# Kernel optimization log

Measured on AMD Instinct MI355X. Metric: run time of the kernel, lower is better.

The kernel has to match this reference:

```python
import jax, jax.numpy as jnp
import numpy as np

B, S, D = 4, 2048, 1024

def setup_inputs() -> dict:
    key = jax.random.key(0)
    ks = jax.random.split(key, 9)
    q = jax.random.normal(ks[0], (B, S, D), dtype=jnp.float32)
    k = jax.random.normal(ks[1], (B, S, D), dtype=jnp.float32)
    v = jax.random.normal(ks[2], (B, S, D), dtype=jnp.float32)
    # Dense layer params (Glorot-ish scale), bias included like keras Dense
    sc = 1.0 / np.sqrt(D)
    Wq = jax.random.normal(ks[3], (D, D), dtype=jnp.float32) * sc
    Wk = jax.random.normal(ks[4], (D, D), dtype=jnp.float32) * sc
    Wv = jax.random.normal(ks[5], (D, D), dtype=jnp.float32) * sc
    bq = jnp.zeros((D,), dtype=jnp.float32)
    bk = jnp.zeros((D,), dtype=jnp.float32)
    bv = jnp.zeros((D,), dtype=jnp.float32)
    # causal mask: 1 where attention is forbidden (future positions)
    mask = jnp.triu(jnp.ones((S, S), dtype=jnp.float32), k=1)
    return {"q": q, "k": k, "v": v, "mask": mask,
            "Wq": Wq, "bq": bq, "Wk": Wk, "bk": bk, "Wv": Wv, "bv": bv}

def reference(q, k, v, mask, Wq, bq, Wk, bk, Wv, bv):
    WQ = q @ Wq + bq                      # [B,S,D]
    WK = k @ Wk + bk
    WV = v @ Wv + bv
    d_k = jnp.asarray(WK.shape[-1], dtype=jnp.float32)
    scores = jnp.einsum('bqd,bkd->bqk', WQ, WK) / jnp.sqrt(d_k)  # [B,S,S]
    scores = scores + mask * (-1e9)
    attn = jax.nn.softmax(scores, axis=-1)
    return jnp.einsum('bqk,bkd->bqd', attn, WV)
```

## Files before the change

kernel.cpp:

```cpp
#include <hip/hip_runtime.h>
#include <math.h>

#define S_LEN 2048
#define D_DIM 1024
#define NB    4

typedef __bf16 bf16_t;
typedef __bf16 bf16x8 __attribute__((ext_vector_type(8)));
typedef float  f32x4  __attribute__((ext_vector_type(4)));
typedef unsigned int   u32;
typedef unsigned short u16;
typedef unsigned int   u32x4 __attribute__((ext_vector_type(4)));

#define BM 128
#define BN 128
#define BK 64

__device__ __forceinline__ u16 f2b_bits(float x) {
    bf16_t h = (bf16_t)x;
    return *(u16*)&h;
}

__device__ __forceinline__ void async16(const void* g, void* l) {
    __builtin_amdgcn_global_load_lds(
        (__attribute__((address_space(1))) const void*)g,
        (__attribute__((address_space(3))) void*)l, 16, 0, 0);
}

#define BAR_RAW() asm volatile("s_barrier" ::: "memory")

__device__ __forceinline__ void gemm_bt_core(
    const bf16_t* __restrict__ A, const bf16_t* __restrict__ Bt,
    int lda, int ldb, int m0, int n0, int kTiles, f32x4 (&acc)[4][4])
{
    __shared__ __attribute__((aligned(16))) bf16_t lA[BM * BK];
    __shared__ __attribute__((aligned(16))) bf16_t lB[BN * BK];
    const int t    = threadIdx.x;
    const int w    = t >> 6;
    const int lane = t & 63;
    const int wr   = w >> 1, wc = w & 1;
    const int srow   = lane >> 3;
    const int kb_src = ((lane & 7) ^ (lane >> 3)) * 8;
    const int fr = lane & 15, fq = lane >> 4;
    const int fof0 = (((0 * 4 + fq) ^ (fr & 7)) * 8);
    const int fof1 = (((1 * 4 + fq) ^ (fr & 7)) * 8);
    const bf16_t* paB0 = lA + (wr * 64 + fr) * BK + fof0;
    const bf16_t* paB1 = lA + (wr * 64 + fr) * BK + fof1;
    const bf16_t* pbB0 = lB + (wc * 64 + fr) * BK + fof0;
    const bf16_t* pbB1 = lB + (wc * 64 + fr) * BK + fof1;
    bf16_t* ldsA = lA + (w * 32) * BK;
    bf16_t* ldsB = lB + (w * 32) * BK;
    const bf16_t* gA = A  + (long)(m0 + w * 32 + srow) * lda + kb_src;
    const bf16_t* gB = Bt + (long)(n0 + w * 32 + srow) * ldb + kb_src;

#pragma unroll
    for (int mt = 0; mt < 4; ++mt)
#pragma unroll
        for (int nt = 0; nt < 4; ++nt)
            acc[mt][nt] = f32x4{0.f, 0.f, 0.f, 0.f};

    for (int kt = 0; kt < kTiles; ++kt) {
        const long k0 = (long)kt * BK;
#pragma unroll
        for (int i = 0; i < 4; ++i) {
            async16(gA + k0 + (long)(i * 8) * lda, ldsA + i * 8 * BK);
            async16(gB + k0 + (long)(i * 8) * ldb, ldsB + i * 8 * BK);
        }
        asm volatile("s_waitcnt vmcnt(0)" ::: "memory");
        __syncthreads();
#pragma unroll
        for (int h = 0; h < 2; ++h) {
            const bf16_t* pa = h ? paB1 : paB0;
            const bf16_t* pb = h ? pbB1 : pbB0;
            bf16x8 af[4], bfv[4];
#pragma unroll
            for (int mt = 0; mt < 4; ++mt)
                af[mt] = *(const bf16x8*)(pa + mt * 16 * BK);
#pragma unroll
            for (int nt = 0; nt < 4; ++nt)
                bfv[nt] = *(const bf16x8*)(pb + nt * 16 * BK);
#pragma unroll
            for (int mt = 0; mt < 4; ++mt)
#pragma unroll
                for (int nt = 0; nt < 4; ++nt)
                    acc[mt][nt] = __builtin_amdgcn_mfma_f32_16x16x32_bf16(
                        af[mt], bfv[nt], acc[mt][nt], 0, 0, 0);
        }
        __syncthreads();
    }
}

__device__ __forceinline__ void gemm_bt_dbuf8(
    const bf16_t* __restrict__ A, const bf16_t* __restrict__ Bt,
    int lda, int ldb, int m0, int n0, int kTiles, f32x4 (&acc)[4][2])
{
    __shared__ __attribute__((aligned(16))) bf16_t lA[2][BM * BK];
    __shared__ __attribute__((aligned(16))) bf16_t lB[2][BN * BK];
    const int t    = threadIdx.x;
    const int w    = t >> 6;
    const int lane = t & 63;
    const int wr   = w >> 2, wc = w & 3;
    const int srow   = lane >> 3;
    const int kb_src = ((lane & 7) ^ srow) * 8;
    const int fr = lane & 15, fq = lane >> 4;
    const int fof0 = (((0 * 4 + fq) ^ (fr & 7)) * 8);
    const int fof1 = (((1 * 4 + fq) ^ (fr & 7)) * 8);
    const int aO0 = (wr * 64 + fr) * BK + fof0;
    const int aO1 = (wr * 64 + fr) * BK + fof1;
    const int bO0 = (wc * 32 + fr) * BK + fof0;
    const int bO1 = (wc * 32 + fr) * BK + fof1;
    const int sOf = (w * 8) * BK;
    const bf16_t* gA = A  + (long)(m0 + w * 8 + srow) * lda + kb_src;
    const bf16_t* gB = Bt + (long)(n0 + w * 8 + srow) * ldb + kb_src;

#pragma unroll
    for (int mt = 0; mt < 4; ++mt)
#pragma unroll
        for (int nt = 0; nt < 2; ++nt)
            acc[mt][nt] = f32x4{0.f, 0.f, 0.f, 0.f};

#pragma unroll
    for (int i = 0; i < 2; ++i) {
        async16(gA + (long)(i * 64) * lda, &lA[0][sOf + i * 64 * BK]);
        async16(gB + (long)(i * 64) * ldb, &lB[0][sOf + i * 64 * BK]);
    }

    for (int kt = 0; kt < kTiles; ++kt) {
        const int cur = kt & 1, nxt = cur ^ 1;
        if (kt + 1 < kTiles) {
            const long k1 = (long)(kt + 1) * BK;
#pragma unroll
            for (int i = 0; i < 2; ++i) {
                async16(gA + k1 + (long)(i * 64) * lda, &lA[nxt][sOf + i * 64 * BK]);
                async16(gB + k1 + (long)(i * 64) * ldb, &lB[nxt][sOf + i * 64 * BK]);
            }
            asm volatile("s_waitcnt vmcnt(4)" ::: "memory");
        } else {
            asm volatile("s_waitcnt vmcnt(0)" ::: "memory");
        }
        BAR_RAW();
        const bf16_t* lac = lA[cur];
        const bf16_t* lbc = lB[cur];
#pragma unroll
        for (int h = 0; h < 2; ++h) {
            const bf16_t* pa = lac + (h ? aO1 : aO0);
            const bf16_t* pb = lbc + (h ? bO1 : bO0);
            bf16x8 af[4], bfv[2];
#pragma unroll
            for (int mt = 0; mt < 4; ++mt)
                af[mt] = *(const bf16x8*)(pa + mt * 16 * BK);
#pragma unroll
            for (int nt = 0; nt < 2; ++nt)
                bfv[nt] = *(const bf16x8*)(pb + nt * 16 * BK);
#pragma unroll
            for (int mt = 0; mt < 4; ++mt)
#pragma unroll
                for (int nt = 0; nt < 2; ++nt)
                    acc[mt][nt] = __builtin_amdgcn_mfma_f32_16x16x32_bf16(
                        af[mt], bfv[nt], acc[mt][nt], 0, 0, 0);
        }
        BAR_RAW();
    }
}

__global__ __launch_bounds__(256) void k_f2b(
    const float* __restrict__ q, const float* __restrict__ k,
    const float* __restrict__ v, bf16_t* __restrict__ Xb)
{
    const int z = blockIdx.z;
    const float* src = (z == 0) ? q : ((z == 1) ? k : v);
    bf16_t* dst = Xb + (long)z * ((long)NB * S_LEN * D_DIM);
    const long i = (long)blockIdx.x * blockDim.x + threadIdx.x;
    float4 a = ((const float4*)src)[i];
    u32 lo = (u32)f2b_bits(a.x) | ((u32)f2b_bits(a.y) << 16);
    u32 hi = (u32)f2b_bits(a.z) | ((u32)f2b_bits(a.w) << 16);
    ((uint2*)(dst))[i] = make_uint2(lo, hi);
}

__global__ __launch_bounds__(256) void k_tw(
    const float* __restrict__ Wq, const float* __restrict__ Wk,
    const float* __restrict__ Wv, bf16_t* __restrict__ Wt)
{
    __shared__ u32 tile[64][33];
    const int z = blockIdx.z;
    const float* W = (z == 0) ? Wq : ((z == 1) ? Wk : Wv);
    bf16_t* T = Wt + (long)z * D_DIM * D_DIM;
    const int t = threadIdx.x;
    const int k0 = blockIdx.x * 64, n0 = blockIdx.y * 64;
#pragma unroll
    for (int rr = 0; rr < 4; ++rr) {
        const int kr = (t >> 4) + rr * 16;
        const int nq = (t & 15) * 4;
        float4 f = *(const float4*)(W + (long)(k0 + kr) * D_DIM + n0 + nq);
        tile[kr][(nq >> 1)]     = (u32)f2b_bits(f.x) | ((u32)f2b_bits(f.y) << 16);
        tile[kr][(nq >> 1) + 1] = (u32)f2b_bits(f.z) | ((u32)f2b_bits(f.w) << 16);
    }
    __syncthreads();
#pragma unroll
    for (int rr = 0; rr < 2; ++rr) {
        const int nr = (t >> 3) + rr * 32;
        const int j0 = (t & 7) * 4;
        u32x4 o;
#pragma unroll
        for (int jj = 0; jj < 4; ++jj) {
            const int j = j0 + jj;
            const u32 ua = tile[2 * j][nr >> 1];
            const u32 ub = tile[2 * j + 1][nr >> 1];
            const u32 lo = (nr & 1) ? (ua >> 16) : (ua & 0xffffu);
            const u32 hi = (nr & 1) ? (ub >> 16) : (ub & 0xffffu);
            o[jj] = lo | (hi << 16);
        }
        *(u32x4*)(T + (long)(n0 + nr) * D_DIM + k0 + 2 * j0) = o;
    }
}

__global__ __launch_bounds__(256) void k_tv(
    const bf16_t* __restrict__ PrV, bf16_t* __restrict__ WVt)
{
    __shared__ u32 tile[64][33];
    const int b = blockIdx.z;
    const bf16_t* src = PrV + (long)b * S_LEN * D_DIM;
    bf16_t* dst = WVt + (long)b * D_DIM * S_LEN;
    const int t = threadIdx.x;
    const int d0 = blockIdx.x * 64, s0 = blockIdx.y * 64;
#pragma unroll
    for (int rr = 0; rr < 2; ++rr) {
        const int sr = (t >> 3) + rr * 32;
        const int dp0 = (t & 7) * 4;
        u32x4 u = *(const u32x4*)(src + (long)(s0 + sr) * D_DIM + d0 + 2 * dp0);
#pragma unroll
        for (int q = 0; q < 4; ++q) tile[sr][dp0 + q] = u[q];
    }
    __syncthreads();
#pragma unroll
    for (int rr = 0; rr < 2; ++rr) {
        const int dr = (t >> 3) + rr * 32;
        const int j0 = (t & 7) * 4;
        u32x4 o;
#pragma unroll
        for (int jj = 0; jj < 4; ++jj) {
            const int j = j0 + jj;
            const u32 ua = tile[2 * j][dr >> 1];
            const u32 ub = tile[2 * j + 1][dr >> 1];
            const u32 lo = (dr & 1) ? (ua >> 16) : (ua & 0xffffu);
            const u32 hi = (dr & 1) ? (ub >> 16) : (ub & 0xffffu);
            o[jj] = lo | (hi << 16);
        }
        *(u32x4*)(dst + (long)(d0 + dr) * S_LEN + s0 + 2 * j0) = o;
    }
}

__global__ __launch_bounds__(256) void k_gemm_proj(
    const bf16_t* __restrict__ Xb, const bf16_t* __restrict__ Wt,
    const float* __restrict__ bq, const float* __restrict__ bk,
    const float* __restrict__ bv, bf16_t* __restrict__ Pr)
{
    const int z = blockIdx.z;
    const bf16_t* A  = Xb + (long)z * ((long)NB * S_LEN * D_DIM);
    const bf16_t* Bt = Wt + (long)z * D_DIM * D_DIM;
    bf16_t* C        = Pr + (long)z * ((long)NB * S_LEN * D_DIM);
    const float* bias = (z == 0) ? bq : ((z == 1) ? bk : bv);
    const int m0 = blockIdx.x * BM, n0 = blockIdx.y * BN;
    f32x4 acc[4][4];
    gemm_bt_core(A, Bt, D_DIM, D_DIM, m0, n0, D_DIM / BK, acc);
    const int lane = threadIdx.x & 63, w = threadIdx.x >> 6;
    const int wr = w >> 1, wc = w & 1;
    const int r0 = m0 + wr * 64 + (lane >> 4) * 4;
    const int c0 = n0 + wc * 64 + (lane & 15);
#pragma unroll
    for (int mt = 0; mt < 4; ++mt)
#pragma unroll
        for (int nt = 0; nt < 4; ++nt) {
            const int col = c0 + nt * 16;
            const float bb = bias[col];
#pragma unroll
            for (int r = 0; r < 4; ++r) {
                const int row = r0 + mt * 16 + r;
                C[(long)row * D_DIM + col] = (bf16_t)(acc[mt][nt][r] + bb);
            }
        }
}

__global__ __launch_bounds__(512) void k_gemm_scores(
    const bf16_t* __restrict__ PrQ, const bf16_t* __restrict__ PrK,
    bf16_t* __restrict__ SC)
{
    const int h = blockIdx.x, b = blockIdx.z;
    const int u = (h & 7) * 17 + (h >> 3);
    int ti = (int)((sqrtf(8.0f * (float)u + 1.0f) - 1.0f) * 0.5f);
    while ((ti + 1) * (ti + 2) / 2 <= u) ++ti;
    while (ti * (ti + 1) / 2 > u) --ti;
    const int tj = u - ti * (ti + 1) / 2;
    const bf16_t* A  = PrQ + (long)b * S_LEN * D_DIM;
    const bf16_t* Bt = PrK + (long)b * S_LEN * D_DIM;
    bf16_t* C        = SC  + (long)b * S_LEN * S_LEN;
    const int m0 = ti * BM, n0 = tj * BN;
    f32x4 acc[4][2];
    gemm_bt_dbuf8(A, Bt, D_DIM, D_DIM, m0, n0, D_DIM / BK, acc);
    const int lane = threadIdx.x & 63, w = threadIdx.x >> 6;
    const int wr = w >> 2, wc = w & 3;
    const int r0 = m0 + wr * 64 + (lane >> 4) * 4;
    const int c0 = n0 + wc * 32 + (lane & 15);
#pragma unroll
    for (int mt = 0; mt < 4; ++mt)
#pragma unroll
        for (int nt = 0; nt < 2; ++nt) {
            const int col = c0 + nt * 16;
#pragma unroll
            for (int r = 0; r < 4; ++r) {
                const int row = r0 + mt * 16 + r;
                C[(long)row * S_LEN + col] = (bf16_t)(acc[mt][nt][r] * 0.03125f);
            }
        }
}

__global__ __launch_bounds__(256) void k_softmax(bf16_t* __restrict__ SC)
{
    const int w = threadIdx.x >> 6, lane = threadIdx.x & 63;
    const int i = blockIdx.x * 4 + w;
    const int b = blockIdx.y;
    bf16_t* row = SC + ((long)b * S_LEN + i) * S_LEN;
    const int n    = i + 1;
    const int jend = ((i >> 7) + 1) << 7;
    const int nch  = (jend + 511) >> 9;
    float x[4][8];
    float mx = -1e30f;
#pragma unroll
    for (int c = 0; c < 4; ++c) {
        if (c < nch) {
            bf16x8 vv = *(const bf16x8*)(row + c * 512 + lane * 8);
#pragma unroll
            for (int e = 0; e < 8; ++e) {
                const int j = c * 512 + lane * 8 + e;
                const float f = (j < n) ? (float)vv[e] : -1e30f;
                x[c][e] = f;
                mx = fmaxf(mx, f);
            }
        }
    }
#pragma unroll
    for (int d = 1; d < 64; d <<= 1) mx = fmaxf(mx, __shfl_xor(mx, d, 64));
    float sm = 0.f;
#pragma unroll
    for (int c = 0; c < 4; ++c) {
        if (c < nch) {
#pragma unroll
            for (int e = 0; e < 8; ++e) {
                const int j = c * 512 + lane * 8 + e;
                float p = (j < n) ? __expf(x[c][e] - mx) : 0.f;
                x[c][e] = p;
                sm += p;
            }
        }
    }
#pragma unroll
    for (int d = 1; d < 64; d <<= 1) sm += __shfl_xor(sm, d, 64);
    const float inv = 1.0f / sm;
#pragma unroll
    for (int c = 0; c < 4; ++c) {
        if (c < nch) {
            bf16x8 o;
#pragma unroll
            for (int e = 0; e < 8; ++e) o[e] = (bf16_t)(x[c][e] * inv);
            *(bf16x8*)(row + c * 512 + lane * 8) = o;
        }
    }
}

__global__ __launch_bounds__(512) void k_gemm_pv(
    const bf16_t* __restrict__ SC, const bf16_t* __restrict__ WVt,
    float* __restrict__ Out)
{
    const int h = blockIdx.x, b = blockIdx.z;
    const int xcd = h & 7, s = h >> 3;
    const int ti  = (s < 8) ? (15 - xcd) : xcd;
    const int n0i = s & 7;
    const bf16_t* A  = SC  + (long)b * S_LEN * S_LEN;
    const bf16_t* Bt = WVt + (long)b * D_DIM * S_LEN;
    float* C         = Out + (long)b * S_LEN * D_DIM;
    const int m0 = ti * BM, n0 = n0i * BN;
    f32x4 acc[4][2];
    gemm_bt_dbuf8(A, Bt, S_LEN, S_LEN, m0, n0, (ti + 1) * (BM / BK), acc);
    const int lane = threadIdx.x & 63, w = threadIdx.x >> 6;
    const int wr = w >> 2, wc = w & 3;
    const int r0 = m0 + wr * 64 + (lane >> 4) * 4;
    const int c0 = n0 + wc * 32 + (lane & 15);
#pragma unroll
    for (int mt = 0; mt < 4; ++mt)
#pragma unroll
        for (int nt = 0; nt < 2; ++nt) {
            const int col = c0 + nt * 16;
#pragma unroll
            for (int r = 0; r < 4; ++r) {
                const int row = r0 + mt * 16 + r;
                C[(long)row * D_DIM + col] = acc[mt][nt][r];
            }
        }
}

extern "C" void kernel_launch(void* const* d_in, const int* in_sizes, int n_in,
                              void* d_out, int out_size, void* d_ws, size_t ws_size,
                              hipStream_t stream)
{
    (void)in_sizes; (void)n_in; (void)out_size; (void)ws_size;
    const float* q  = (const float*)d_in[0];
    const float* k  = (const float*)d_in[1];
    const float* v  = (const float*)d_in[2];
    const float* Wq = (const float*)d_in[4];
    const float* bq = (const float*)d_in[5];
    const float* Wk = (const float*)d_in[6];
    const float* bk = (const float*)d_in[7];
    const float* Wv = (const float*)d_in[8];
    const float* bv = (const float*)d_in[9];
    float* out = (float*)d_out;

    bf16_t* ws = (bf16_t*)d_ws;
    const long nW = (long)D_DIM * D_DIM;
    const long nX = (long)NB * S_LEN * D_DIM;
    bf16_t* Wt  = ws;
    bf16_t* Xb  = Wt + 3 * nW;
    bf16_t* SC  = Xb;
    bf16_t* Pr  = Xb + 3 * nX;
    bf16_t* WVt = Pr + 3 * nX;
    bf16_t* PrQ = Pr;
    bf16_t* PrK = Pr + nX;
    bf16_t* PrV = Pr + 2 * nX;

    k_f2b        <<<dim3(8192, 1, 3),   256, 0, stream>>>(q, k, v, Xb);
    k_tw         <<<dim3(16, 16, 3),    256, 0, stream>>>(Wq, Wk, Wv, Wt);
    k_gemm_proj  <<<dim3(64, 8, 3),     256, 0, stream>>>(Xb, Wt, bq, bk, bv, Pr);
    k_tv         <<<dim3(16, 32, NB),   256, 0, stream>>>(PrV, WVt);
    k_gemm_scores<<<dim3(136, 1, NB),   512, 0, stream>>>(PrQ, PrK, SC);
    k_softmax    <<<dim3(S_LEN / 4, NB),256, 0, stream>>>(SC);
    k_gemm_pv    <<<dim3(128, 1, NB),   512, 0, stream>>>(SC, WVt, out);
}
```

Before: 299.2 us.

## Merge independent prep kernels into combined launches with shared LDS buffer

Folds the f32-to-bf16 input conversion and the weight transpose into one kernel (k_pre), and the V transpose into the QK scores GEMM kernel (k_mid), dispatching work by block index. Launches drop from seven to five, and independent work can overlap instead of serializing on kernel boundaries. The GEMM helper now takes a caller-provided LDS buffer so transpose blocks can reuse the same shared memory. In exchange, the light transpose blocks now carry the GEMM kernel's large LDS allocation, which may reduce how many can be resident at once.

```diff
diff --git a/kernel.cpp b/kernel.cpp
--- a/kernel.cpp
+++ b/kernel.cpp
@@ -90,12 +90,13 @@
     }
 }
 
-__device__ __forceinline__ void gemm_bt_dbuf8(
+__device__ __forceinline__ void gemm_bt_dbuf8_p(
+    bf16_t* __restrict__ lds,
     const bf16_t* __restrict__ A, const bf16_t* __restrict__ Bt,
     int lda, int ldb, int m0, int n0, int kTiles, f32x4 (&acc)[4][2])
 {
-    __shared__ __attribute__((aligned(16))) bf16_t lA[2][BM * BK];
-    __shared__ __attribute__((aligned(16))) bf16_t lB[2][BN * BK];
+    bf16_t* lAb[2] = { lds,         lds + 8192  };
+    bf16_t* lBb[2] = { lds + 16384, lds + 24576 };
     const int t    = threadIdx.x;
     const int w    = t >> 6;
     const int lane = t & 63;
@@ -121,8 +122,8 @@
 
 #pragma unroll
     for (int i = 0; i < 2; ++i) {
-        async16(gA + (long)(i * 64) * lda, &lA[0][sOf + i * 64 * BK]);
-        async16(gB + (long)(i * 64) * ldb, &lB[0][sOf + i * 64 * BK]);
+        async16(gA + (long)(i * 64) * lda, lAb[0] + sOf + i * 64 * BK);
+        async16(gB + (long)(i * 64) * ldb, lBb[0] + sOf + i * 64 * BK);
     }
 
     for (int kt = 0; kt < kTiles; ++kt) {
@@ -131,16 +132,16 @@
             const long k1 = (long)(kt + 1) * BK;
 #pragma unroll
             for (int i = 0; i < 2; ++i) {
-                async16(gA + k1 + (long)(i * 64) * lda, &lA[nxt][sOf + i * 64 * BK]);
-                async16(gB + k1 + (long)(i * 64) * ldb, &lB[nxt][sOf + i * 64 * BK]);
+                async16(gA + k1 + (long)(i * 64) * lda, lAb[nxt] + sOf + i * 64 * BK);
+                async16(gB + k1 + (long)(i * 64) * ldb, lBb[nxt] + sOf + i * 64 * BK);
             }
             asm volatile("s_waitcnt vmcnt(4)" ::: "memory");
         } else {
             asm volatile("s_waitcnt vmcnt(0)" ::: "memory");
         }
         BAR_RAW();
-        const bf16_t* lac = lA[cur];
-        const bf16_t* lbc = lB[cur];
+        const bf16_t* lac = lAb[cur];
+        const bf16_t* lbc = lBb[cur];
 #pragma unroll
         for (int h = 0; h < 2; ++h) {
             const bf16_t* pa = lac + (h ? aO1 : aO0);
@@ -163,30 +164,28 @@
     }
 }
 
-__global__ __launch_bounds__(256) void k_f2b(
+__global__ __launch_bounds__(256) void k_pre(
     const float* __restrict__ q, const float* __restrict__ k,
-    const float* __restrict__ v, bf16_t* __restrict__ Xb)
-{
-    const int z = blockIdx.z;
-    const float* src = (z == 0) ? q : ((z == 1) ? k : v);
-    bf16_t* dst = Xb + (long)z * ((long)NB * S_LEN * D_DIM);
-    const long i = (long)blockIdx.x * blockDim.x + threadIdx.x;
-    float4 a = ((const float4*)src)[i];
-    u32 lo = (u32)f2b_bits(a.x) | ((u32)f2b_bits(a.y) << 16);
-    u32 hi = (u32)f2b_bits(a.z) | ((u32)f2b_bits(a.w) << 16);
-    ((uint2*)(dst))[i] = make_uint2(lo, hi);
-}
-
-__global__ __launch_bounds__(256) void k_tw(
+    const float* __restrict__ v, bf16_t* __restrict__ Xb,
     const float* __restrict__ Wq, const float* __restrict__ Wk,
     const float* __restrict__ Wv, bf16_t* __restrict__ Wt)
 {
     __shared__ u32 tile[64][33];
-    const int z = blockIdx.z;
+    const int z = blockIdx.z, bx = blockIdx.x, t = threadIdx.x;
+    if (bx < 8192) {
+        const float* src = (z == 0) ? q : ((z == 1) ? k : v);
+        bf16_t* dst = Xb + (long)z * ((long)NB * S_LEN * D_DIM);
+        const long i = (long)bx * 256 + t;
+        float4 a = ((const float4*)src)[i];
+        u32 lo = (u32)f2b_bits(a.x) | ((u32)f2b_bits(a.y) << 16);
+        u32 hi = (u32)f2b_bits(a.z) | ((u32)f2b_bits(a.w) << 16);
+        ((uint2*)(dst))[i] = make_uint2(lo, hi);
+        return;
+    }
+    const int u = bx - 8192;
     const float* W = (z == 0) ? Wq : ((z == 1) ? Wk : Wv);
     bf16_t* T = Wt + (long)z * D_DIM * D_DIM;
-    const int t = threadIdx.x;
-    const int k0 = blockIdx.x * 64, n0 = blockIdx.y * 64;
+    const int k0 = (u >> 4) * 64, n0 = (u & 15) * 64;
 #pragma unroll
     for (int rr = 0; rr < 4; ++rr) {
         const int kr = (t >> 4) + rr * 16;
@@ -211,42 +210,6 @@
             o[jj] = lo | (hi << 16);
         }
         *(u32x4*)(T + (long)(n0 + nr) * D_DIM + k0 + 2 * j0) = o;
-    }
-}
-
-__global__ __launch_bounds__(256) void k_tv(
-    const bf16_t* __restrict__ PrV, bf16_t* __restrict__ WVt)
-{
-    __shared__ u32 tile[64][33];
-    const int b = blockIdx.z;
-    const bf16_t* src = PrV + (long)b * S_LEN * D_DIM;
-    bf16_t* dst = WVt + (long)b * D_DIM * S_LEN;
-    const int t = threadIdx.x;
-    const int d0 = blockIdx.x * 64, s0 = blockIdx.y * 64;
-#pragma unroll
-    for (int rr = 0; rr < 2; ++rr) {
-        const int sr = (t >> 3) + rr * 32;
-        const int dp0 = (t & 7) * 4;
-        u32x4 u = *(const u32x4*)(src + (long)(s0 + sr) * D_DIM + d0 + 2 * dp0);
-#pragma unroll
-        for (int q = 0; q < 4; ++q) tile[sr][dp0 + q] = u[q];
-    }
-    __syncthreads();
-#pragma unroll
-    for (int rr = 0; rr < 2; ++rr) {
-        const int dr = (t >> 3) + rr * 32;
-        const int j0 = (t & 7) * 4;
-        u32x4 o;
-#pragma unroll
-        for (int jj = 0; jj < 4; ++jj) {
-            const int j = j0 + jj;
-            const u32 ua = tile[2 * j][dr >> 1];
-            const u32 ub = tile[2 * j + 1][dr >> 1];
-            const u32 lo = (dr & 1) ? (ua >> 16) : (ua & 0xffffu);
-            const u32 hi = (dr & 1) ? (ub >> 16) : (ub & 0xffffu);
-            o[jj] = lo | (hi << 16);
-        }
-        *(u32x4*)(dst + (long)(d0 + dr) * S_LEN + s0 + 2 * j0) = o;
     }
 }
 
@@ -281,37 +244,76 @@
         }
 }
 
-__global__ __launch_bounds__(512) void k_gemm_scores(
+__global__ __launch_bounds__(512) void k_mid(
     const bf16_t* __restrict__ PrQ, const bf16_t* __restrict__ PrK,
-    bf16_t* __restrict__ SC)
-{
-    const int h = blockIdx.x, b = blockIdx.z;
-    const int u = (h & 7) * 17 + (h >> 3);
-    int ti = (int)((sqrtf(8.0f * (float)u + 1.0f) - 1.0f) * 0.5f);
-    while ((ti + 1) * (ti + 2) / 2 <= u) ++ti;
-    while (ti * (ti + 1) / 2 > u) --ti;
-    const int tj = u - ti * (ti + 1) / 2;
-    const bf16_t* A  = PrQ + (long)b * S_LEN * D_DIM;
-    const bf16_t* Bt = PrK + (long)b * S_LEN * D_DIM;
-    bf16_t* C        = SC  + (long)b * S_LEN * S_LEN;
-    const int m0 = ti * BM, n0 = tj * BN;
-    f32x4 acc[4][2];
-    gemm_bt_dbuf8(A, Bt, D_DIM, D_DIM, m0, n0, D_DIM / BK, acc);
-    const int lane = threadIdx.x & 63, w = threadIdx.x >> 6;
-    const int wr = w >> 2, wc = w & 3;
-    const int r0 = m0 + wr * 64 + (lane >> 4) * 4;
-    const int c0 = n0 + wc * 32 + (lane & 15);
-#pragma unroll
-    for (int mt = 0; mt < 4; ++mt)
-#pragma unroll
-        for (int nt = 0; nt < 2; ++nt) {
-            const int col = c0 + nt * 16;
-#pragma unroll
-            for (int r = 0; r < 4; ++r) {
-                const int row = r0 + mt * 16 + r;
-                C[(long)row * S_LEN + col] = (bf16_t)(acc[mt][nt][r] * 0.03125f);
-            }
-        }
+    bf16_t* __restrict__ SC,
+    const bf16_t* __restrict__ PrV, bf16_t* __restrict__ WVt)
+{
+    __shared__ __attribute__((aligned(16))) bf16_t smem[32768];
+    const int bx = blockIdx.x, b = blockIdx.z, t = threadIdx.x;
+    if (bx < 136) {
+        const int u = (bx & 7) * 17 + (bx >> 3);
+        int ti = (int)((sqrtf(8.0f * (float)u + 1.0f) - 1.0f) * 0.5f);
+        while ((ti + 1) * (ti + 2) / 2 <= u) ++ti;
+        while (ti * (ti + 1) / 2 > u) --ti;
+        const int tj = u - ti * (ti + 1) / 2;
+        const bf16_t* A  = PrQ + (long)b * S_LEN * D_DIM;
+        const bf16_t* Bt = PrK + (long)b * S_LEN * D_DIM;
+        bf16_t* C        = SC  + (long)b * S_LEN * S_LEN;
+        const int m0 = ti * BM, n0 = tj * BN;
+        f32x4 acc[4][2];
+        gemm_bt_dbuf8_p(smem, A, Bt, D_DIM, D_DIM, m0, n0, D_DIM / BK, acc);
+        const int lane = t & 63, w = t >> 6;
+        const int wr = w >> 2, wc = w & 3;
+        const int r0 = m0 + wr * 64 + (lane >> 4) * 4;
+        const int c0 = n0 + wc * 32 + (lane & 15);
+#pragma unroll
+        for (int mt = 0; mt < 4; ++mt)
+#pragma unroll
+            for (int nt = 0; nt < 2; ++nt) {
+                const int col = c0 + nt * 16;
+#pragma unroll
+                for (int r = 0; r < 4; ++r) {
+                    const int row = r0 + mt * 16 + r;
+                    C[(long)row * S_LEN + col] = (bf16_t)(acc[mt][nt][r] * 0.03125f);
+                }
+            }
+        return;
+    }
+    const int u2   = bx - 136;
+    const int half = t >> 8;
+    const int tl   = t & 255;
+    const int ti2  = u2 * 2 + half;
+    const int d0 = (ti2 >> 5) * 64, s0 = (ti2 & 31) * 64;
+    const bf16_t* src = PrV + (long)b * S_LEN * D_DIM;
+    bf16_t* dst = WVt + (long)b * D_DIM * S_LEN;
+    u32* tb = (u32*)smem;
+    u32 (*tile)[33] = (u32(*)[33])(tb + half * 64 * 33);
+#pragma unroll
+    for (int rr = 0; rr < 2; ++rr) {
+        const int sr = (tl >> 3) + rr * 32;
+        const int dp0 = (tl & 7) * 4;
+        u32x4 uu = *(const u32x4*)(src + (long)(s0 + sr) * D_DIM + d0 + 2 * dp0);
+#pragma unroll
+        for (int qq = 0; qq < 4; ++qq) tile[sr][dp0 + qq] = uu[qq];
+    }
+    __syncthreads();
+#pragma unroll
+    for (int rr = 0; rr < 2; ++rr) {
+        const int dr = (tl >> 3) + rr * 32;
+        const int j0 = (tl & 7) * 4;
+        u32x4 o;
+#pragma unroll
+        for (int jj = 0; jj < 4; ++jj) {
+            const int j = j0 + jj;
+            const u32 ua = tile[2 * j][dr >> 1];
+            const u32 ub = tile[2 * j + 1][dr >> 1];
+            const u32 lo = (dr & 1) ? (ua >> 16) : (ua & 0xffffu);
+            const u32 hi = (dr & 1) ? (ub >> 16) : (ub & 0xffffu);
+            o[jj] = lo | (hi << 16);
+        }
+        *(u32x4*)(dst + (long)(d0 + dr) * S_LEN + s0 + 2 * j0) = o;
+    }
 }
 
 __global__ __launch_bounds__(256) void k_softmax(bf16_t* __restrict__ SC)
@@ -371,6 +373,7 @@
     const bf16_t* __restrict__ SC, const bf16_t* __restrict__ WVt,
     float* __restrict__ Out)
 {
+    __shared__ __attribute__((aligned(16))) bf16_t smem[32768];
     const int h = blockIdx.x, b = blockIdx.z;
     const int xcd = h & 7, s = h >> 3;
     const int ti  = (s < 8) ? (15 - xcd) : xcd;
@@ -380,7 +383,7 @@
     float* C         = Out + (long)b * S_LEN * D_DIM;
     const int m0 = ti * BM, n0 = n0i * BN;
     f32x4 acc[4][2];
-    gemm_bt_dbuf8(A, Bt, S_LEN, S_LEN, m0, n0, (ti + 1) * (BM / BK), acc);
+    gemm_bt_dbuf8_p(smem, A, Bt, S_LEN, S_LEN, m0, n0, (ti + 1) * (BM / BK), acc);
     const int lane = threadIdx.x & 63, w = threadIdx.x >> 6;
     const int wr = w >> 2, wc = w & 3;
     const int r0 = m0 + wr * 64 + (lane >> 4) * 4;
@@ -426,11 +429,9 @@
     bf16_t* PrK = Pr + nX;
     bf16_t* PrV = Pr + 2 * nX;
 
-    k_f2b        <<<dim3(8192, 1, 3),   256, 0, stream>>>(q, k, v, Xb);
-    k_tw         <<<dim3(16, 16, 3),    256, 0, stream>>>(Wq, Wk, Wv, Wt);
+    k_pre        <<<dim3(8448, 1, 3),   256, 0, stream>>>(q, k, v, Xb, Wq, Wk, Wv, Wt);
     k_gemm_proj  <<<dim3(64, 8, 3),     256, 0, stream>>>(Xb, Wt, bq, bk, bv, Pr);
-    k_tv         <<<dim3(16, 32, NB),   256, 0, stream>>>(PrV, WVt);
-    k_gemm_scores<<<dim3(136, 1, NB),   512, 0, stream>>>(PrQ, PrK, SC);
+    k_mid        <<<dim3(392, 1, NB),   512, 0, stream>>>(PrQ, PrK, SC, PrV, WVt);
     k_softmax    <<<dim3(S_LEN / 4, NB),256, 0, stream>>>(SC);
     k_gemm_pv    <<<dim3(128, 1, NB),   512, 0, stream>>>(SC, WVt, out);
 }
```

Result: slower. 347.0 us (+16.0%).

## Split-K the long PV rows and switch GEMM core to single-buffered LDS

Applied to the files above, without the earlier changes.

The causal PV GEMM is rebalanced by splitting the longest row tiles (rows 1024-2047) into two K halves. Each half writes to its own buffer, and a new merge kernel adds the partial result into the output, so that block work is more even across the grid. The shared GEMM helper used by both scores and PV is also changed from double-buffered to single-buffered LDS with a full vmcnt(0) wait. This halves LDS use per block but removes the overlap between loads and MFMA. The extra partial buffer, reusing the projection workspace, and the added merge launch add memory traffic.

```diff
diff --git a/kernel.cpp b/kernel.cpp
--- a/kernel.cpp
+++ b/kernel.cpp
@@ -26,8 +26,6 @@
         (__attribute__((address_space(1))) const void*)g,
         (__attribute__((address_space(3))) void*)l, 16, 0, 0);
 }
-
-#define BAR_RAW() asm volatile("s_barrier" ::: "memory")
 
 __device__ __forceinline__ void gemm_bt_core(
     const bf16_t* __restrict__ A, const bf16_t* __restrict__ Bt,
@@ -90,12 +88,12 @@
     }
 }
 
-__device__ __forceinline__ void gemm_bt_dbuf8(
+__device__ __forceinline__ void gemm_bt_sbuf8(
     const bf16_t* __restrict__ A, const bf16_t* __restrict__ Bt,
     int lda, int ldb, int m0, int n0, int kTiles, f32x4 (&acc)[4][2])
 {
-    __shared__ __attribute__((aligned(16))) bf16_t lA[2][BM * BK];
-    __shared__ __attribute__((aligned(16))) bf16_t lB[2][BN * BK];
+    __shared__ __attribute__((aligned(16))) bf16_t lA[BM * BK];
+    __shared__ __attribute__((aligned(16))) bf16_t lB[BN * BK];
     const int t    = threadIdx.x;
     const int w    = t >> 6;
     const int lane = t & 63;
@@ -119,32 +117,19 @@
         for (int nt = 0; nt < 2; ++nt)
             acc[mt][nt] = f32x4{0.f, 0.f, 0.f, 0.f};
 
-#pragma unroll
-    for (int i = 0; i < 2; ++i) {
-        async16(gA + (long)(i * 64) * lda, &lA[0][sOf + i * 64 * BK]);
-        async16(gB + (long)(i * 64) * ldb, &lB[0][sOf + i * 64 * BK]);
-    }
-
     for (int kt = 0; kt < kTiles; ++kt) {
-        const int cur = kt & 1, nxt = cur ^ 1;
-        if (kt + 1 < kTiles) {
-            const long k1 = (long)(kt + 1) * BK;
-#pragma unroll
-            for (int i = 0; i < 2; ++i) {
-                async16(gA + k1 + (long)(i * 64) * lda, &lA[nxt][sOf + i * 64 * BK]);
-                async16(gB + k1 + (long)(i * 64) * ldb, &lB[nxt][sOf + i * 64 * BK]);
-            }
-            asm volatile("s_waitcnt vmcnt(4)" ::: "memory");
-        } else {
-            asm volatile("s_waitcnt vmcnt(0)" ::: "memory");
-        }
-        BAR_RAW();
-        const bf16_t* lac = lA[cur];
-        const bf16_t* lbc = lB[cur];
+        const long k0 = (long)kt * BK;
+#pragma unroll
+        for (int i = 0; i < 2; ++i) {
+            async16(gA + k0 + (long)(i * 64) * lda, lA + sOf + i * 64 * BK);
+            async16(gB + k0 + (long)(i * 64) * ldb, lB + sOf + i * 64 * BK);
+        }
+        asm volatile("s_waitcnt vmcnt(0)" ::: "memory");
+        __syncthreads();
 #pragma unroll
         for (int h = 0; h < 2; ++h) {
-            const bf16_t* pa = lac + (h ? aO1 : aO0);
-            const bf16_t* pb = lbc + (h ? bO1 : bO0);
+            const bf16_t* pa = lA + (h ? aO1 : aO0);
+            const bf16_t* pb = lB + (h ? bO1 : bO0);
             bf16x8 af[4], bfv[2];
 #pragma unroll
             for (int mt = 0; mt < 4; ++mt)
@@ -159,7 +144,7 @@
                     acc[mt][nt] = __builtin_amdgcn_mfma_f32_16x16x32_bf16(
                         af[mt], bfv[nt], acc[mt][nt], 0, 0, 0);
         }
-        BAR_RAW();
+        __syncthreads();
     }
 }
 
@@ -296,7 +281,7 @@
     bf16_t* C        = SC  + (long)b * S_LEN * S_LEN;
     const int m0 = ti * BM, n0 = tj * BN;
     f32x4 acc[4][2];
-    gemm_bt_dbuf8(A, Bt, D_DIM, D_DIM, m0, n0, D_DIM / BK, acc);
+    gemm_bt_sbuf8(A, Bt, D_DIM, D_DIM, m0, n0, D_DIM / BK, acc);
     const int lane = threadIdx.x & 63, w = threadIdx.x >> 6;
     const int wr = w >> 2, wc = w & 3;
     const int r0 = m0 + wr * 64 + (lane >> 4) * 4;
@@ -369,33 +354,77 @@
 
 __global__ __launch_bounds__(512) void k_gemm_pv(
     const bf16_t* __restrict__ SC, const bf16_t* __restrict__ WVt,
-    float* __restrict__ Out)
-{
-    const int h = blockIdx.x, b = blockIdx.z;
-    const int xcd = h & 7, s = h >> 3;
-    const int ti  = (s < 8) ? (15 - xcd) : xcd;
-    const int n0i = s & 7;
-    const bf16_t* A  = SC  + (long)b * S_LEN * S_LEN;
-    const bf16_t* Bt = WVt + (long)b * D_DIM * S_LEN;
-    float* C         = Out + (long)b * S_LEN * D_DIM;
+    float* __restrict__ Out, float* __restrict__ Out2)
+{
+    const int bx = blockIdx.x;
+    int ti, n0i, b, ktn, second;
+    long kofs;
+    if (bx < 512) {
+        ti = 15 - (bx >> 6);
+        const int rem = bx & 63;
+        b   = rem >> 4;
+        n0i = (rem >> 1) & 7;
+        const int chunk = rem & 1;
+        ktn  = ti + 1;
+        kofs = (long)chunk * ktn * BK;
+        second = chunk;
+    } else {
+        const int l = bx - 512;
+        ti = 7 - (l >> 5);
+        const int rem = l & 31;
+        b   = rem >> 3;
+        n0i = rem & 7;
+        ktn  = (ti + 1) * 2;
+        kofs = 0;
+        second = 0;
+    }
+    const bf16_t* A  = SC  + (long)b * S_LEN * S_LEN + kofs;
+    const bf16_t* Bt = WVt + (long)b * D_DIM * S_LEN + kofs;
     const int m0 = ti * BM, n0 = n0i * BN;
     f32x4 acc[4][2];
-    gemm_bt_dbuf8(A, Bt, S_LEN, S_LEN, m0, n0, (ti + 1) * (BM / BK), acc);
+    gemm_bt_sbuf8(A, Bt, S_LEN, S_LEN, m0, n0, ktn, acc);
     const int lane = threadIdx.x & 63, w = threadIdx.x >> 6;
     const int wr = w >> 2, wc = w & 3;
     const int r0 = m0 + wr * 64 + (lane >> 4) * 4;
     const int c0 = n0 + wc * 32 + (lane & 15);
-#pragma unroll
-    for (int mt = 0; mt < 4; ++mt)
-#pragma unroll
-        for (int nt = 0; nt < 2; ++nt) {
-            const int col = c0 + nt * 16;
-#pragma unroll
-            for (int r = 0; r < 4; ++r) {
-                const int row = r0 + mt * 16 + r;
-                C[(long)row * D_DIM + col] = acc[mt][nt][r];
-            }
-        }
+    if (second) {
+        float* O2 = Out2 + (long)b * 1024 * D_DIM;
+#pragma unroll
+        for (int mt = 0; mt < 4; ++mt)
+#pragma unroll
+            for (int nt = 0; nt < 2; ++nt) {
+                const int col = c0 + nt * 16;
+#pragma unroll
+                for (int r = 0; r < 4; ++r) {
+                    const int row = r0 + mt * 16 + r;
+                    O2[(long)(row - 1024) * D_DIM + col] = acc[mt][nt][r];
+                }
+            }
+    } else {
+        float* C = Out + (long)b * S_LEN * D_DIM;
+#pragma unroll
+        for (int mt = 0; mt < 4; ++mt)
+#pragma unroll
+            for (int nt = 0; nt < 2; ++nt) {
+                const int col = c0 + nt * 16;
+#pragma unroll
+                for (int r = 0; r < 4; ++r) {
+                    const int row = r0 + mt * 16 + r;
+                    C[(long)row * D_DIM + col] = acc[mt][nt][r];
+                }
+            }
+    }
+}
+
+__global__ __launch_bounds__(256) void k_merge(
+    float* __restrict__ Out, const float* __restrict__ Out2)
+{
+    const int b = blockIdx.y, r = blockIdx.x, t = threadIdx.x;
+    float4* o = (float4*)(Out + ((long)b * S_LEN + 1024 + r) * D_DIM) + t;
+    const float4* p = (const float4*)(Out2 + (long)b * 1024 * D_DIM
+                                      + (long)r * D_DIM) + t;
+    float4 a = *o, c = *p;
+    *o = make_float4(a.x + c.x, a.y + c.y, a.z + c.z, a.w + c.w);
 }
 
 extern "C" void kernel_launch(void* const* d_in, const int* in_sizes, int n_in,
@@ -425,6 +454,7 @@
     bf16_t* PrQ = Pr;
     bf16_t* PrK = Pr + nX;
     bf16_t* PrV = Pr + 2 * nX;
+    float*  Out2 = (float*)Pr;
 
     k_f2b        <<<dim3(8192, 1, 3),   256, 0, stream>>>(q, k, v, Xb);
     k_tw         <<<dim3(16, 16, 3),    256, 0, stream>>>(Wq, Wk, Wv, Wt);
@@ -432,5 +462,6 @@
     k_tv         <<<dim3(16, 32, NB),   256, 0, stream>>>(PrV, WVt);
     k_gemm_scores<<<dim3(136, 1, NB),   512, 0, stream>>>(PrQ, PrK, SC);
     k_softmax    <<<dim3(S_LEN / 4, NB),256, 0, stream>>>(SC);
-    k_gemm_pv    <<<dim3(128, 1, NB),   512, 0, stream>>>(SC, WVt, out);
-}
+    k_gemm_pv    <<<dim3(768, 1, 1),    512, 0, stream>>>(SC, WVt, out, Out2);
+    k_merge      <<<dim3(1024, NB),     256, 0, stream>>>(out, Out2);
+}
```

After: 300.3 us. Within noise of the previous version (+0.4%).
